# Kernel tuning notes

Measured on AMD Instinct MI355X. Metric: run time of the kernel, lower is better.

## Reference

```python
import jax, jax.numpy as jnp
import numpy as np

B, S, E, H = 2, 2048, 1024, 16  # batch, max_seq_length, embedding_dim, num_heads
D = E // H  # head dim = 64


def setup_inputs() -> dict:
    key = jax.random.key(0)
    ks = jax.random.split(key, 7)
    scale = 0.02
    return {
        "inputs": jax.random.normal(ks[0], (B, S, E), jnp.float32),
        "embbeding_V": jax.random.normal(ks[1], (B, S, E), jnp.float32),
        "embbeding_K": jax.random.normal(ks[2], (B, S, E), jnp.float32),
        "Wq": jax.random.normal(ks[3], (E, E), jnp.float32) * scale,
        "Wk": jax.random.normal(ks[4], (E, E), jnp.float32) * scale,
        "Wv": jax.random.normal(ks[5], (E, E), jnp.float32) * scale,
        "Wo": jax.random.normal(ks[6], (E, E), jnp.float32) * scale,
    }


def reference(inputs, embbeding_V, embbeding_K, Wq, Wk, Wv, Wo):
    b = inputs.shape[0]
    # repeat last token of `inputs` to max_seq_length: [b, S, E]
    x = jnp.broadcast_to(inputs[:, -1, :][:, None, :], (b, S, E))
    # torch Linear(bias=False): y = x @ W.T ; split heads -> [b, H, S, D]
    q = (x @ Wq.T).reshape(b, S, H, D).transpose(0, 2, 1, 3)
    k = (embbeding_K @ Wk.T).reshape(b, S, H, D).transpose(0, 2, 1, 3)
    v = (embbeding_V @ Wv.T).reshape(b, S, H, D).transpose(0, 2, 1, 3)
    # UNSCALED attention (faithful to source: no 1/sqrt(d))
    s = jnp.einsum("bhqd,bhkd->bhqk", q, k)
    p = jax.nn.softmax(s, axis=-1)
    o = jnp.einsum("bhqk,bhkd->bhqd", p, v)
    # transpose(1,2) then reshape to [b, S, E]
    o = o.transpose(0, 2, 1, 3).reshape(b, S, E)
    return o @ Wo.T
```

## Files before the change

### kernel.cpp

```cpp
#include <hip/hip_runtime.h>

constexpr int B = 2, S = 2048, E = 1024, H = 16, D = 64;
constexpr int E4 = E / 4;

__device__ __forceinline__ float dot4(float4 a, float4 w) {
  return a.x * w.x + a.y * w.y + a.z * w.z + a.w * w.w;
}

__global__ void k_qvec(const float4* __restrict__ x, const float4* __restrict__ Wq,
                       float* __restrict__ q_vec) {
  int blk = blockIdx.x;
  int b = blk >> 7, n0 = (blk & 127) * 8;
  int tid = threadIdx.x;
  int nl = tid >> 5, es = tid & 31;
  const float4* xr = x + ((size_t)b * S + (S - 1)) * E4;
  const float4* wr = Wq + (size_t)(n0 + nl) * E4;
  float acc = 0.f;
#pragma unroll
  for (int j = 0; j < 8; ++j) {
    float4 a = xr[es + 32 * j];
    float4 w = wr[es + 32 * j];
    acc += dot4(a, w);
  }
#pragma unroll
  for (int o = 16; o > 0; o >>= 1) acc += __shfl_xor(acc, o, 64);
  if (es == 0) q_vec[b * E + n0 + nl] = acc;
}

__global__ __launch_bounds__(256) void k_wkq(const float* __restrict__ q_vec,
                                             const float4* __restrict__ Wk4,
                                             float4* __restrict__ wkq4,
                                             float* __restrict__ rowsum) {
  int bb = blockIdx.x;
  int bh = bb >> 3, eo = bb & 7;
  int b = bh >> 4, h = bh & 15;
  int tid = threadIdx.x;
  __shared__ float qh[D];
  __shared__ float4 red4[256];
  if (tid < D) qh[tid] = q_vec[b * E + h * D + tid];
  if (eo == 0 && tid == 0) rowsum[bh] = 0.f;
  __syncthreads();
  int dq = tid >> 5, el = tid & 31;
  int e4 = eo * 32 + el;
  float4 acc = make_float4(0.f, 0.f, 0.f, 0.f);
#pragma unroll
  for (int i = 0; i < 8; ++i) {
    int d = dq * 8 + i;
    float qd = qh[d];
    float4 wk = Wk4[(size_t)(h * D + d) * E4 + e4];
    acc.x += qd * wk.x; acc.y += qd * wk.y; acc.z += qd * wk.z; acc.w += qd * wk.w;
  }
  red4[dq * 32 + el] = acc;
  __syncthreads();
  if (tid < 32) {
    float4 r = make_float4(0.f, 0.f, 0.f, 0.f);
#pragma unroll
    for (int g = 0; g < 8; ++g) {
      float4 c = red4[g * 32 + tid];
      r.x += c.x; r.y += c.y; r.z += c.z; r.w += c.w;
    }
    wkq4[(size_t)bh * E4 + eo * 32 + tid] = r;
  }
}

__global__ __launch_bounds__(256) void k_scores_exp(const float4* __restrict__ embK,
                                                    const float4* __restrict__ wkq4,
                                                    float* __restrict__ p,
                                                    float* __restrict__ rowsum) {
  __shared__ float4 wl4[H * E4];
  __shared__ float hsum[16];
  int bb = blockIdx.x;
  int b = bb >> 8, k0 = (bb & 255) * 8;
  int tid = threadIdx.x;
  const float4* wsrc = wkq4 + (size_t)b * (H * E4);
#pragma unroll
  for (int j = 0; j < 16; ++j) wl4[j * 256 + tid] = wsrc[j * 256 + tid];
  if (tid < 16) hsum[tid] = 0.f;
  __syncthreads();
  int wv = tid >> 6, lane = tid & 63;
  const float4* e0 = embK + ((size_t)b * S + k0 + wv) * E4;
  const float4* e1 = embK + ((size_t)b * S + k0 + wv + 4) * E4;
  float4 va[4], vb[4];
#pragma unroll
  for (int j = 0; j < 4; ++j) { va[j] = e0[lane + 64 * j]; vb[j] = e1[lane + 64 * j]; }
#pragma unroll 1
  for (int h = 0; h < H; ++h) {
    float a0 = 0.f, a1 = 0.f;
#pragma unroll
    for (int j = 0; j < 4; ++j) {
      float4 w = wl4[h * 256 + lane + 64 * j];
      a0 += dot4(va[j], w); a1 += dot4(vb[j], w);
    }
#pragma unroll
    for (int o = 32; o > 0; o >>= 1) {
      a0 += __shfl_xor(a0, o, 64); a1 += __shfl_xor(a1, o, 64);
    }
    if (lane == 0) {
      float p0 = __expf(a0), p1 = __expf(a1);
      float* pr = p + ((size_t)(b * H + h)) * S + k0 + wv;
      pr[0] = p0; pr[4] = p1;
      atomicAdd(&hsum[h], p0 + p1);
    }
  }
  __syncthreads();
  if (tid < 16) atomicAdd(&rowsum[b * H + tid], hsum[tid]);
}

__global__ __launch_bounds__(256) void k_ctx_part(const float4* __restrict__ embV,
                                                  const float* __restrict__ p,
                                                  float4* __restrict__ part) {
  int b = blockIdx.x, eo = blockIdx.y, kz = blockIdx.z;
  int tid = threadIdx.x;
  int k0 = kz * 256;
  __shared__ float pl[16 * 256];
  __shared__ float4 red4[4 * 16 * 16];
  for (int i = tid; i < 16 * 256; i += 256) {
    pl[i] = p[((size_t)(b * H + (i >> 8))) * S + k0 + (i & 255)];
  }
  __syncthreads();
  const float4* pl4 = (const float4*)pl;
  int e4l = tid & 15, ks = tid >> 4;
  int e4 = eo * 16 + e4l;
  float4 acc[H];
#pragma unroll
  for (int h = 0; h < H; ++h) acc[h] = make_float4(0.f, 0.f, 0.f, 0.f);
#pragma unroll
  for (int i4 = 0; i4 < 4; ++i4) {
    int kk = ks * 16 + i4 * 4;
    const float4* vbp = embV + ((size_t)b * S + k0 + kk) * E4 + e4;
    float4 v0 = vbp[0 * E4], v1 = vbp[1 * E4], v2 = vbp[2 * E4], v3 = vbp[3 * E4];
    int kq = kk >> 2;
#pragma unroll
    for (int h = 0; h < H; ++h) {
      float4 p4 = pl4[h * 64 + kq];
      acc[h].x += p4.x * v0.x + p4.y * v1.x + p4.z * v2.x + p4.w * v3.x;
      acc[h].y += p4.x * v0.y + p4.y * v1.y + p4.z * v2.y + p4.w * v3.y;
      acc[h].z += p4.x * v0.z + p4.y * v1.z + p4.z * v2.z + p4.w * v3.z;
      acc[h].w += p4.x * v0.w + p4.y * v1.w + p4.z * v2.w + p4.w * v3.w;
    }
  }
  int lane = tid & 63, wv = tid >> 6;
#pragma unroll
  for (int h = 0; h < H; ++h) {
    acc[h].x += __shfl_xor(acc[h].x, 16, 64); acc[h].y += __shfl_xor(acc[h].y, 16, 64);
    acc[h].z += __shfl_xor(acc[h].z, 16, 64); acc[h].w += __shfl_xor(acc[h].w, 16, 64);
    acc[h].x += __shfl_xor(acc[h].x, 32, 64); acc[h].y += __shfl_xor(acc[h].y, 32, 64);
    acc[h].z += __shfl_xor(acc[h].z, 32, 64); acc[h].w += __shfl_xor(acc[h].w, 32, 64);
  }
  if (lane < 16) {
#pragma unroll
    for (int h = 0; h < H; ++h) red4[(wv * 16 + h) * 16 + lane] = acc[h];
  }
  __syncthreads();
  {
    int h = tid >> 4, el = tid & 15;
    float4 r = make_float4(0.f, 0.f, 0.f, 0.f);
#pragma unroll
    for (int ww = 0; ww < 4; ++ww) {
      float4 c = red4[(ww * 16 + h) * 16 + el];
      r.x += c.x; r.y += c.y; r.z += c.z; r.w += c.w;
    }
    part[((size_t)(kz * B + b) * H + h) * E4 + eo * 16 + el] = r;
  }
}

__global__ __launch_bounds__(256) void k_red_ov(const float4* __restrict__ part,
                                                const float4* __restrict__ Wv4,
                                                const float* __restrict__ rowsum,
                                                float* __restrict__ o_vec) {
  int bb = blockIdx.x;
  int bh = bb >> 1, half = bb & 1;
  int b = bh >> 4, h = bh & 15;
  int tid = threadIdx.x;
  __shared__ float4 ctxl[E4];
  {
    const size_t pstride = (size_t)B * H * E4;
    const float4* pp = part + ((size_t)b * H + h) * E4 + tid;
    float4 r = make_float4(0.f, 0.f, 0.f, 0.f);
#pragma unroll
    for (int pz = 0; pz < 8; ++pz) {
      float4 c = pp[pz * pstride];
      r.x += c.x; r.y += c.y; r.z += c.z; r.w += c.w;
    }
    ctxl[tid] = r;
  }
  __syncthreads();
  int wv = tid >> 6, lane = tid & 63;
  float inv_rs = rowsum[bh];
#pragma unroll 1
  for (int i = 0; i < 8; ++i) {
    int n = h * D + half * 32 + wv * 8 + i;
    const float4* wr = Wv4 + (size_t)n * E4;
    float acc = 0.f;
#pragma unroll
    for (int j = 0; j < 4; ++j) acc += dot4(ctxl[lane + 64 * j], wr[lane + 64 * j]);
#pragma unroll
    for (int o = 32; o > 0; o >>= 1) acc += __shfl_xor(acc, o, 64);
    if (lane == 0) o_vec[b * E + n] = acc / inv_rs;
  }
}

__global__ void k_outvec(const float* __restrict__ o_vec, const float4* __restrict__ Wo4,
                         float* __restrict__ out_vec) {
  int gw = (blockIdx.x * blockDim.x + threadIdx.x) >> 6;
  int lane = threadIdx.x & 63;
  int b = gw >> 10, nn = gw & 1023;
  const float4* xr = (const float4*)(o_vec + (size_t)b * E);
  const float4* wr = Wo4 + (size_t)nn * E4;
  float acc = 0.f;
#pragma unroll
  for (int j = 0; j < 4; ++j) {
    float4 a = xr[lane + 64 * j];
    float4 w = wr[lane + 64 * j];
    acc += dot4(a, w);
  }
#pragma unroll
  for (int o = 32; o > 0; o >>= 1) acc += __shfl_xor(acc, o, 64);
  if (lane == 0) out_vec[gw] = acc;
}

__global__ void k_bcast(const float4* __restrict__ ov4, float4* __restrict__ out4) {
  int base = blockIdx.x * 1024 + threadIdx.x;
#pragma unroll
  for (int r = 0; r < 4; ++r) {
    int g = base + r * 256;
    out4[g] = ov4[(g >> 19) * E4 + (g & 255)];
  }
}

extern "C" void kernel_launch(void* const* d_in, const int* in_sizes, int n_in,
                              void* d_out, int out_size, void* d_ws, size_t ws_size,
                              hipStream_t stream) {
  const float* inputs = (const float*)d_in[0];
  const float* embV   = (const float*)d_in[1];
  const float* embK   = (const float*)d_in[2];
  const float* Wq     = (const float*)d_in[3];
  const float* Wk     = (const float*)d_in[4];
  const float* Wv     = (const float*)d_in[5];
  const float* Wo     = (const float*)d_in[6];

  float* ws      = (float*)d_ws;
  float* q_vec   = ws;
  float* wkq     = q_vec + B * E;
  float* p       = wkq + B * H * E;
  float* rowsum  = p + B * H * S;
  float* o_vec   = rowsum + 64;
  float* out_vec = o_vec + B * E;
  float* part    = out_vec + B * E;

  k_qvec<<<256, 256, 0, stream>>>((const float4*)inputs, (const float4*)Wq, q_vec);
  k_wkq<<<256, 256, 0, stream>>>(q_vec, (const float4*)Wk, (float4*)wkq, rowsum);
  k_scores_exp<<<512, 256, 0, stream>>>((const float4*)embK, (const float4*)wkq,
                                        p, rowsum);
  k_ctx_part<<<dim3(B, 16, 8), 256, 0, stream>>>((const float4*)embV, p, (float4*)part);
  k_red_ov<<<64, 256, 0, stream>>>((const float4*)part, (const float4*)Wv, rowsum, o_vec);
  k_outvec<<<512, 256, 0, stream>>>(o_vec, (const float4*)Wo, out_vec);
  k_bcast<<<1024, 256, 0, stream>>>((const float4*)out_vec, (float4*)d_out);
}
```

Measured before the change: 137.3 us.

## Fuse q-projection into Wk fold and output projection into broadcast

Merges the q-vector projection and the Wk·q fold into one kernel per (batch, head), and fuses the Wo output projection with the broadcast write so each block recomputes its 128 output columns and writes them across 256 rows. This cuts the launch count from seven to five and drops the q_vec and out_vec round trips through global memory. In exchange the fused qwk kernel runs on only 32 blocks, which leaves most of the GPU idle for that stage. The output kernel also recomputes the Wo GEMV eight times redundantly, once per sequence chunk.

New measurement: 157.7 us. 1.15x slower.

```diff
diff --git a/kernel.cpp b/kernel.cpp
--- a/kernel.cpp
+++ b/kernel.cpp
@@ -7,59 +7,42 @@
   return a.x * w.x + a.y * w.y + a.z * w.z + a.w * w.w;
 }
 
-__global__ void k_qvec(const float4* __restrict__ x, const float4* __restrict__ Wq,
-                       float* __restrict__ q_vec) {
-  int blk = blockIdx.x;
-  int b = blk >> 7, n0 = (blk & 127) * 8;
-  int tid = threadIdx.x;
-  int nl = tid >> 5, es = tid & 31;
-  const float4* xr = x + ((size_t)b * S + (S - 1)) * E4;
-  const float4* wr = Wq + (size_t)(n0 + nl) * E4;
-  float acc = 0.f;
-#pragma unroll
-  for (int j = 0; j < 8; ++j) {
-    float4 a = xr[es + 32 * j];
-    float4 w = wr[es + 32 * j];
-    acc += dot4(a, w);
-  }
-#pragma unroll
-  for (int o = 16; o > 0; o >>= 1) acc += __shfl_xor(acc, o, 64);
-  if (es == 0) q_vec[b * E + n0 + nl] = acc;
-}
-
-__global__ __launch_bounds__(256) void k_wkq(const float* __restrict__ q_vec,
+__global__ __launch_bounds__(256) void k_qwk(const float4* __restrict__ x,
+                                             const float4* __restrict__ Wq4,
                                              const float4* __restrict__ Wk4,
                                              float4* __restrict__ wkq4,
                                              float* __restrict__ rowsum) {
-  int bb = blockIdx.x;
-  int bh = bb >> 3, eo = bb & 7;
+  int bh = blockIdx.x;
   int b = bh >> 4, h = bh & 15;
   int tid = threadIdx.x;
   __shared__ float qh[D];
-  __shared__ float4 red4[256];
-  if (tid < D) qh[tid] = q_vec[b * E + h * D + tid];
-  if (eo == 0 && tid == 0) rowsum[bh] = 0.f;
-  __syncthreads();
-  int dq = tid >> 5, el = tid & 31;
-  int e4 = eo * 32 + el;
-  float4 acc = make_float4(0.f, 0.f, 0.f, 0.f);
-#pragma unroll
-  for (int i = 0; i < 8; ++i) {
-    int d = dq * 8 + i;
-    float qd = qh[d];
-    float4 wk = Wk4[(size_t)(h * D + d) * E4 + e4];
-    acc.x += qd * wk.x; acc.y += qd * wk.y; acc.z += qd * wk.z; acc.w += qd * wk.w;
-  }
-  red4[dq * 32 + el] = acc;
-  __syncthreads();
-  if (tid < 32) {
-    float4 r = make_float4(0.f, 0.f, 0.f, 0.f);
-#pragma unroll
-    for (int g = 0; g < 8; ++g) {
-      float4 c = red4[g * 32 + tid];
-      r.x += c.x; r.y += c.y; r.z += c.z; r.w += c.w;
-    }
-    wkq4[(size_t)bh * E4 + eo * 32 + tid] = r;
+  if (tid == 0) rowsum[bh] = 0.f;
+  {
+    int g = tid >> 5, es = tid & 31;
+    const float4* xr = x + ((size_t)b * S + (S - 1)) * E4;
+#pragma unroll 1
+    for (int dd = 0; dd < 8; ++dd) {
+      int d = dd * 8 + g;
+      const float4* wr = Wq4 + (size_t)(h * D + d) * E4;
+      float acc = 0.f;
+#pragma unroll
+      for (int j = 0; j < 8; ++j) acc += dot4(xr[es + 32 * j], wr[es + 32 * j]);
+#pragma unroll
+      for (int o = 16; o > 0; o >>= 1) acc += __shfl_xor(acc, o, 64);
+      if (es == 0) qh[d] = acc;
+    }
+  }
+  __syncthreads();
+  {
+    float4 acc = make_float4(0.f, 0.f, 0.f, 0.f);
+    const float4* wkp = Wk4 + (size_t)(h * D) * E4 + tid;
+#pragma unroll 8
+    for (int d = 0; d < D; ++d) {
+      float qd = qh[d];
+      float4 wk = wkp[(size_t)d * E4];
+      acc.x += qd * wk.x; acc.y += qd * wk.y; acc.z += qd * wk.z; acc.w += qd * wk.w;
+    }
+    wkq4[(size_t)bh * E4 + tid] = acc;
   }
 }
 
@@ -186,7 +169,7 @@
   }
   __syncthreads();
   int wv = tid >> 6, lane = tid & 63;
-  float inv_rs = rowsum[bh];
+  float rs = rowsum[bh];
 #pragma unroll 1
   for (int i = 0; i < 8; ++i) {
     int n = h * D + half * 32 + wv * 8 + i;
@@ -196,35 +179,40 @@
     for (int j = 0; j < 4; ++j) acc += dot4(ctxl[lane + 64 * j], wr[lane + 64 * j]);
 #pragma unroll
     for (int o = 32; o > 0; o >>= 1) acc += __shfl_xor(acc, o, 64);
-    if (lane == 0) o_vec[b * E + n] = acc / inv_rs;
-  }
-}
-
-__global__ void k_outvec(const float* __restrict__ o_vec, const float4* __restrict__ Wo4,
-                         float* __restrict__ out_vec) {
-  int gw = (blockIdx.x * blockDim.x + threadIdx.x) >> 6;
-  int lane = threadIdx.x & 63;
-  int b = gw >> 10, nn = gw & 1023;
-  const float4* xr = (const float4*)(o_vec + (size_t)b * E);
-  const float4* wr = Wo4 + (size_t)nn * E4;
-  float acc = 0.f;
-#pragma unroll
-  for (int j = 0; j < 4; ++j) {
-    float4 a = xr[lane + 64 * j];
-    float4 w = wr[lane + 64 * j];
-    acc += dot4(a, w);
-  }
-#pragma unroll
-  for (int o = 32; o > 0; o >>= 1) acc += __shfl_xor(acc, o, 64);
-  if (lane == 0) out_vec[gw] = acc;
-}
-
-__global__ void k_bcast(const float4* __restrict__ ov4, float4* __restrict__ out4) {
-  int base = blockIdx.x * 1024 + threadIdx.x;
-#pragma unroll
-  for (int r = 0; r < 4; ++r) {
-    int g = base + r * 256;
-    out4[g] = ov4[(g >> 19) * E4 + (g & 255)];
+    if (lane == 0) o_vec[b * E + n] = acc / rs;
+  }
+}
+
+__global__ __launch_bounds__(256) void k_out_bcast(const float4* __restrict__ ov4,
+                                                   const float4* __restrict__ Wo4,
+                                                   float4* __restrict__ out4) {
+  int b = blockIdx.x, sz = blockIdx.y, nz = blockIdx.z;
+  int s0 = sz * 256, n0 = nz * 128;
+  int tid = threadIdx.x;
+  __shared__ float4 ovl[E4];
+  __shared__ float outl[128];
+  ovl[tid] = ov4[(size_t)b * E4 + tid];
+  __syncthreads();
+  int wv = tid >> 6, lane = tid & 63;
+#pragma unroll 1
+  for (int i = 0; i < 32; ++i) {
+    int n = n0 + wv * 32 + i;
+    const float4* wr = Wo4 + (size_t)n * E4;
+    float acc = 0.f;
+#pragma unroll
+    for (int j = 0; j < 4; ++j) acc += dot4(ovl[lane + 64 * j], wr[lane + 64 * j]);
+#pragma unroll
+    for (int o = 32; o > 0; o >>= 1) acc += __shfl_xor(acc, o, 64);
+    if (lane == 0) outl[wv * 32 + i] = acc;
+  }
+  __syncthreads();
+  const float4* outl4 = (const float4*)outl;
+  int col = tid & 31, rsub = tid >> 5;
+  float4 val = outl4[col];
+#pragma unroll
+  for (int it = 0; it < 32; ++it) {
+    int row = s0 + it * 8 + rsub;
+    out4[((size_t)(b * S + row)) * E4 + nz * 32 + col] = val;
   }
 }
 
@@ -240,20 +228,18 @@
   const float* Wo     = (const float*)d_in[6];
 
   float* ws      = (float*)d_ws;
-  float* q_vec   = ws;
-  float* wkq     = q_vec + B * E;
+  float* wkq     = ws;
   float* p       = wkq + B * H * E;
   float* rowsum  = p + B * H * S;
   float* o_vec   = rowsum + 64;
-  float* out_vec = o_vec + B * E;
-  float* part    = out_vec + B * E;
-
-  k_qvec<<<256, 256, 0, stream>>>((const float4*)inputs, (const float4*)Wq, q_vec);
-  k_wkq<<<256, 256, 0, stream>>>(q_vec, (const float4*)Wk, (float4*)wkq, rowsum);
+  float* part    = o_vec + B * E;
+
+  k_qwk<<<32, 256, 0, stream>>>((const float4*)inputs, (const float4*)Wq,
+                                (const float4*)Wk, (float4*)wkq, rowsum);
   k_scores_exp<<<512, 256, 0, stream>>>((const float4*)embK, (const float4*)wkq,
                                         p, rowsum);
   k_ctx_part<<<dim3(B, 16, 8), 256, 0, stream>>>((const float4*)embV, p, (float4*)part);
   k_red_ov<<<64, 256, 0, stream>>>((const float4*)part, (const float4*)Wv, rowsum, o_vec);
-  k_outvec<<<512, 256, 0, stream>>>(o_vec, (const float4*)Wo, out_vec);
-  k_bcast<<<1024, 256, 0, stream>>>((const float4*)out_vec, (float4*)d_out);
-}
+  k_out_bcast<<<dim3(B, 8, 8), 256, 0, stream>>>((const float4*)o_vec,
+                                                 (const float4*)Wo, (float4*)d_out);
+}
```

## Atomic ctx accumulation, split Wv projection widely, fuse Wo projection with broadcast

Applied to the files above, without the earlier changes.

Context partials are now summed with float atomicAdds into a ctx buffer that k_qvec zeroes, which removes the separate partial-reduction pass. The Wv projection moves to a 512-block wave-per-output kernel in place of the 64-block one. The Wo projection is fused with the output broadcast, so each block recomputes its 64 output columns and writes 128 rows, removing a launch and the out_vec round trip. The cost is atomic contention, nondeterministic summation order, and redundant Wo GEMV work repeated across the 16 sequence tiles.

After: 143.1 us. +4.3%, slower.

```diff
diff --git a/kernel.cpp b/kernel.cpp
--- a/kernel.cpp
+++ b/kernel.cpp
@@ -8,10 +8,12 @@
 }
 
 __global__ void k_qvec(const float4* __restrict__ x, const float4* __restrict__ Wq,
-                       float* __restrict__ q_vec) {
+                       float* __restrict__ q_vec, float4* __restrict__ ctx4) {
   int blk = blockIdx.x;
   int b = blk >> 7, n0 = (blk & 127) * 8;
   int tid = threadIdx.x;
+  int gid = blk * 256 + tid;
+  if (gid < B * H * E4) ctx4[gid] = make_float4(0.f, 0.f, 0.f, 0.f);
   int nl = tid >> 5, es = tid & 31;
   const float4* xr = x + ((size_t)b * S + (S - 1)) * E4;
   const float4* wr = Wq + (size_t)(n0 + nl) * E4;
@@ -106,9 +108,9 @@
   if (tid < 16) atomicAdd(&rowsum[b * H + tid], hsum[tid]);
 }
 
-__global__ __launch_bounds__(256) void k_ctx_part(const float4* __restrict__ embV,
-                                                  const float* __restrict__ p,
-                                                  float4* __restrict__ part) {
+__global__ __launch_bounds__(256) void k_ctx_atomic(const float4* __restrict__ embV,
+                                                    const float* __restrict__ p,
+                                                    float* __restrict__ ctx) {
   int b = blockIdx.x, eo = blockIdx.y, kz = blockIdx.z;
   int tid = threadIdx.x;
   int k0 = kz * 256;
@@ -160,53 +162,20 @@
       float4 c = red4[(ww * 16 + h) * 16 + el];
       r.x += c.x; r.y += c.y; r.z += c.z; r.w += c.w;
     }
-    part[((size_t)(kz * B + b) * H + h) * E4 + eo * 16 + el] = r;
-  }
-}
-
-__global__ __launch_bounds__(256) void k_red_ov(const float4* __restrict__ part,
-                                                const float4* __restrict__ Wv4,
-                                                const float* __restrict__ rowsum,
-                                                float* __restrict__ o_vec) {
-  int bb = blockIdx.x;
-  int bh = bb >> 1, half = bb & 1;
-  int b = bh >> 4, h = bh & 15;
-  int tid = threadIdx.x;
-  __shared__ float4 ctxl[E4];
-  {
-    const size_t pstride = (size_t)B * H * E4;
-    const float4* pp = part + ((size_t)b * H + h) * E4 + tid;
-    float4 r = make_float4(0.f, 0.f, 0.f, 0.f);
-#pragma unroll
-    for (int pz = 0; pz < 8; ++pz) {
-      float4 c = pp[pz * pstride];
-      r.x += c.x; r.y += c.y; r.z += c.z; r.w += c.w;
-    }
-    ctxl[tid] = r;
-  }
-  __syncthreads();
-  int wv = tid >> 6, lane = tid & 63;
-  float inv_rs = rowsum[bh];
-#pragma unroll 1
-  for (int i = 0; i < 8; ++i) {
-    int n = h * D + half * 32 + wv * 8 + i;
-    const float4* wr = Wv4 + (size_t)n * E4;
-    float acc = 0.f;
-#pragma unroll
-    for (int j = 0; j < 4; ++j) acc += dot4(ctxl[lane + 64 * j], wr[lane + 64 * j]);
-#pragma unroll
-    for (int o = 32; o > 0; o >>= 1) acc += __shfl_xor(acc, o, 64);
-    if (lane == 0) o_vec[b * E + n] = acc / inv_rs;
-  }
-}
-
-__global__ void k_outvec(const float* __restrict__ o_vec, const float4* __restrict__ Wo4,
-                         float* __restrict__ out_vec) {
+    float* cp = ctx + (((size_t)(b * H + h)) * E4 + eo * 16 + el) * 4;
+    atomicAdd(cp + 0, r.x); atomicAdd(cp + 1, r.y);
+    atomicAdd(cp + 2, r.z); atomicAdd(cp + 3, r.w);
+  }
+}
+
+__global__ void k_ov(const float* __restrict__ ctx, const float4* __restrict__ Wv4,
+                     const float* __restrict__ rowsum, float* __restrict__ o_vec) {
   int gw = (blockIdx.x * blockDim.x + threadIdx.x) >> 6;
   int lane = threadIdx.x & 63;
   int b = gw >> 10, nn = gw & 1023;
-  const float4* xr = (const float4*)(o_vec + (size_t)b * E);
-  const float4* wr = Wo4 + (size_t)nn * E4;
+  int bh = b * H + (nn >> 6);
+  const float4* xr = (const float4*)(ctx + (size_t)bh * E);
+  const float4* wr = Wv4 + (size_t)nn * E4;
   float acc = 0.f;
 #pragma unroll
   for (int j = 0; j < 4; ++j) {
@@ -216,15 +185,39 @@
   }
 #pragma unroll
   for (int o = 32; o > 0; o >>= 1) acc += __shfl_xor(acc, o, 64);
-  if (lane == 0) out_vec[gw] = acc;
-}
-
-__global__ void k_bcast(const float4* __restrict__ ov4, float4* __restrict__ out4) {
-  int base = blockIdx.x * 1024 + threadIdx.x;
-#pragma unroll
-  for (int r = 0; r < 4; ++r) {
-    int g = base + r * 256;
-    out4[g] = ov4[(g >> 19) * E4 + (g & 255)];
+  if (lane == 0) o_vec[gw] = acc / rowsum[bh];
+}
+
+__global__ __launch_bounds__(256) void k_out_bcast(const float4* __restrict__ ov4,
+                                                   const float4* __restrict__ Wo4,
+                                                   float4* __restrict__ out4) {
+  int b = blockIdx.x, sz = blockIdx.y, nz = blockIdx.z;
+  int s0 = sz * 128, n0 = nz * 64;
+  int tid = threadIdx.x;
+  __shared__ float4 ovl[E4];
+  __shared__ float outl[64];
+  ovl[tid] = ov4[(size_t)b * E4 + tid];
+  __syncthreads();
+  int wv = tid >> 6, lane = tid & 63;
+#pragma unroll 1
+  for (int i = 0; i < 16; ++i) {
+    int n = n0 + wv * 16 + i;
+    const float4* wr = Wo4 + (size_t)n * E4;
+    float acc = 0.f;
+#pragma unroll
+    for (int j = 0; j < 4; ++j) acc += dot4(ovl[lane + 64 * j], wr[lane + 64 * j]);
+#pragma unroll
+    for (int o = 32; o > 0; o >>= 1) acc += __shfl_xor(acc, o, 64);
+    if (lane == 0) outl[wv * 16 + i] = acc;
+  }
+  __syncthreads();
+  const float4* outl4 = (const float4*)outl;
+  int col = tid & 15, rsub = tid >> 4;
+  float4 val = outl4[col];
+#pragma unroll
+  for (int it = 0; it < 8; ++it) {
+    int row = s0 + it * 16 + rsub;
+    out4[((size_t)(b * S + row)) * E4 + nz * 16 + col] = val;
   }
 }
 
@@ -245,15 +238,15 @@
   float* p       = wkq + B * H * E;
   float* rowsum  = p + B * H * S;
   float* o_vec   = rowsum + 64;
-  float* out_vec = o_vec + B * E;
-  float* part    = out_vec + B * E;
-
-  k_qvec<<<256, 256, 0, stream>>>((const float4*)inputs, (const float4*)Wq, q_vec);
+  float* ctx     = o_vec + B * E;
+
+  k_qvec<<<256, 256, 0, stream>>>((const float4*)inputs, (const float4*)Wq,
+                                  q_vec, (float4*)ctx);
   k_wkq<<<256, 256, 0, stream>>>(q_vec, (const float4*)Wk, (float4*)wkq, rowsum);
   k_scores_exp<<<512, 256, 0, stream>>>((const float4*)embK, (const float4*)wkq,
                                         p, rowsum);
-  k_ctx_part<<<dim3(B, 16, 8), 256, 0, stream>>>((const float4*)embV, p, (float4*)part);
-  k_red_ov<<<64, 256, 0, stream>>>((const float4*)part, (const float4*)Wv, rowsum, o_vec);
-  k_outvec<<<512, 256, 0, stream>>>(o_vec, (const float4*)Wo, out_vec);
-  k_bcast<<<1024, 256, 0, stream>>>((const float4*)out_vec, (float4*)d_out);
-}
+  k_ctx_atomic<<<dim3(B, 16, 8), 256, 0, stream>>>((const float4*)embV, p, ctx);
+  k_ov<<<512, 256, 0, stream>>>(ctx, (const float4*)Wv, rowsum, o_vec);
+  k_out_bcast<<<dim3(B, 16, 16), 256, 0, stream>>>((const float4*)o_vec,
+                                                   (const float4*)Wo, (float4*)d_out);
+}
```
